# Kernel tuning notes

Measured on AMD Instinct MI355X. Metric: run time of the kernel, lower is better.

Reference implementation:

```python
import jax, jax.numpy as jnp
import numpy as np

B, S, H, NH = 4, 2048, 1024, 16
HD = H // NH
SCALE = 1.0 / np.sqrt(HD)
MASK_VAL = -1e9  # fp32 branch of the torch code


def setup_inputs() -> dict:
    key = jax.random.key(0)
    ks = jax.random.split(key, 6)
    s = 1.0 / np.sqrt(H)
    return {
        "x": jax.random.normal(ks[0], (B, S, H), dtype=jnp.float32),
        "attention_mask": jnp.ones((B, S), dtype=jnp.int32),
        "Wq": jax.random.normal(ks[1], (H, H), dtype=jnp.float32) * s,
        "Wk": jax.random.normal(ks[2], (H, H), dtype=jnp.float32) * s,
        "Wv": jax.random.normal(ks[3], (H, H), dtype=jnp.float32) * s,
        "Wo": jax.random.normal(ks[4], (H, H), dtype=jnp.float32) * s,
        "bo": jnp.zeros((H,), dtype=jnp.float32),
    }


def reference(x, attention_mask, Wq, Wk, Wv, Wo, bo):
    b, s, h = x.shape
    # projections; torch Linear computes x @ W.T
    q = (x @ Wq.T).reshape(b, s, NH, HD).transpose(0, 2, 1, 3)  # [b,nh,s,hd]
    k = (x @ Wk.T).reshape(b, s, NH, HD).transpose(0, 2, 1, 3)
    v = (x @ Wv.T).reshape(b, s, NH, HD).transpose(0, 2, 1, 3)

    scores = jnp.einsum("bhqd,bhkd->bhqk", q, k) * SCALE  # [b,nh,s,s]
    # padding mask: [b,1,1,s]
    pad = (attention_mask == 0)[:, None, None, :]
    scores = jnp.where(pad, MASK_VAL, scores)
    # causal mask
    causal = jnp.tril(jnp.ones((s, s), dtype=bool))[None, None]
    scores = jnp.where(causal, scores, MASK_VAL)

    attn = jax.nn.softmax(scores, axis=-1)  # dropout p=0 / eval -> identity
    out = jnp.einsum("bhqk,bhkd->bhqd", attn, v)
    out = out.transpose(0, 2, 1, 3).reshape(b, s, h)
    return out @ Wo.T + bo
```

## Files before the change

### kernel.cpp

```cpp
#include <hip/hip_runtime.h>

#define B_ 4
#define S_ 2048
#define H_ 1024
#define NH_ 16
#define HD_ 64
#define QSCALE_ 0.1803368801111204f

typedef __attribute__((ext_vector_type(8))) short bf16x8;
typedef __attribute__((ext_vector_type(4))) float f32x4;
typedef __attribute__((ext_vector_type(16))) float f32x16;

__device__ __forceinline__ unsigned short f2bf(float f) {
    unsigned u = __float_as_uint(f);
    unsigned r = (u + 0x7FFFu + ((u >> 16) & 1u)) >> 16;
    return (unsigned short)r;
}
__device__ __forceinline__ float exp2f_hw(float x) { return __builtin_amdgcn_exp2f(x); }

__global__ __launch_bounds__(256) void cast_f32_bf16(const float* __restrict__ in,
                                                     unsigned short* __restrict__ out, int n4) {
    int i = blockIdx.x * 256 + threadIdx.x;
    if (i < n4) {
        float4 v = reinterpret_cast<const float4*>(in)[i];
        ushort4 o;
        o.x = f2bf(v.x); o.y = f2bf(v.y); o.z = f2bf(v.z); o.w = f2bf(v.w);
        reinterpret_cast<ushort4*>(out)[i] = o;
    }
}

__device__ __forceinline__ void stage128_swz(const char* g, int gstride, char* lds, int tid) {
    int wave = tid >> 6, lane = tid & 63;
#pragma unroll
    for (int j = 0; j < 4; ++j) {
        int o = ((wave * 4 + j) * 64 + lane) * 16;
        int r = o >> 7;
        int slot = (o >> 4) & 7;
        const char* src = g + (size_t)r * gstride + ((slot ^ (r & 7)) << 4);
        __builtin_amdgcn_global_load_lds((const __attribute__((address_space(1))) void*)src,
                                         (__attribute__((address_space(3))) void*)(lds + (wave * 4 + j) * 1024),
                                         16, 0, 0);
    }
}
__device__ __forceinline__ void stage64_swz(const char* g, int gstride, char* lds, int tid) {
    int wave = tid >> 6, lane = tid & 63;
#pragma unroll
    for (int j = 0; j < 2; ++j) {
        int o = ((wave * 2 + j) * 64 + lane) * 16;
        int r = o >> 7;
        int slot = (o >> 4) & 7;
        const char* src = g + (size_t)r * gstride + ((slot ^ (r & 7)) << 4);
        __builtin_amdgcn_global_load_lds((const __attribute__((address_space(1))) void*)src,
                                         (__attribute__((address_space(3))) void*)(lds + (wave * 2 + j) * 1024),
                                         16, 0, 0);
    }
}

__device__ __forceinline__ bf16x8 frag_swz(const char* lds, int row, int slot) {
    return *reinterpret_cast<const bf16x8*>(lds + row * 128 + (((slot) ^ (row & 7)) << 4));
}

__global__ __launch_bounds__(256) void gemm_qkv(const unsigned short* __restrict__ xb,
                                                const unsigned short* __restrict__ Wq,
                                                const unsigned short* __restrict__ Wk,
                                                const unsigned short* __restrict__ Wv,
                                                unsigned short* __restrict__ Qo,
                                                unsigned short* __restrict__ Ko,
                                                unsigned short* __restrict__ Vo) {
    __shared__ __align__(16) char As[128 * 128];
    __shared__ __align__(16) char Bs[128 * 128];
    int tid = threadIdx.x, lane = tid & 63, wave = tid >> 6;
    int wr = wave >> 1, wc = wave & 1;
    int brow = blockIdx.x * 128;
    int mat = blockIdx.y >> 3;
    int bcol = (blockIdx.y & 7) * 128;
    const unsigned short* W = mat == 0 ? Wq : (mat == 1 ? Wk : Wv);
    unsigned short* O = mat == 0 ? Qo : (mat == 1 ? Ko : Vo);
    float oscale = (mat == 0) ? QSCALE_ : 1.0f;
    f32x4 acc[4][4] = {};
    const char* ga = (const char*)(xb + (size_t)brow * H_);
    const char* gb = (const char*)(W + (size_t)bcol * H_);
    int ro = lane & 15, kg = lane >> 4;
    for (int kt = 0; kt < H_ / 64; ++kt) {
        stage128_swz(ga + kt * 128, H_ * 2, As, tid);
        stage128_swz(gb + kt * 128, H_ * 2, Bs, tid);
        __syncthreads();
#pragma unroll
        for (int kk = 0; kk < 2; ++kk) {
            bf16x8 af[4], bfr[4];
#pragma unroll
            for (int m = 0; m < 4; ++m) af[m] = frag_swz(As, wr * 64 + m * 16 + ro, kk * 4 + kg);
#pragma unroll
            for (int n = 0; n < 4; ++n) bfr[n] = frag_swz(Bs, wc * 64 + n * 16 + ro, kk * 4 + kg);
#pragma unroll
            for (int m = 0; m < 4; ++m)
#pragma unroll
                for (int n = 0; n < 4; ++n)
                    acc[m][n] = __builtin_amdgcn_mfma_f32_16x16x32_bf16(af[m], bfr[n], acc[m][n], 0, 0, 0);
        }
        __syncthreads();
    }
#pragma unroll
    for (int m = 0; m < 4; ++m)
#pragma unroll
        for (int n = 0; n < 4; ++n)
#pragma unroll
            for (int i = 0; i < 4; ++i) {
                int row = brow + wr * 64 + m * 16 + kg * 4 + i;
                int col = bcol + wc * 64 + n * 16 + ro;
                O[(size_t)row * H_ + col] = f2bf(acc[m][n][i] * oscale);
            }
}

__global__ __launch_bounds__(256) void gemm_out(const unsigned short* __restrict__ Ab,
                                                const unsigned short* __restrict__ Wo,
                                                const float* __restrict__ bo,
                                                float* __restrict__ out) {
    __shared__ __align__(16) char As[128 * 128];
    __shared__ __align__(16) char Bs[128 * 128];
    int tid = threadIdx.x, lane = tid & 63, wave = tid >> 6;
    int wr = wave >> 1, wc = wave & 1;
    int brow = blockIdx.x * 128;
    int bcol = blockIdx.y * 128;
    f32x4 acc[4][4] = {};
    const char* ga = (const char*)(Ab + (size_t)brow * H_);
    const char* gb = (const char*)(Wo + (size_t)bcol * H_);
    int ro = lane & 15, kg = lane >> 4;
    for (int kt = 0; kt < H_ / 64; ++kt) {
        stage128_swz(ga + kt * 128, H_ * 2, As, tid);
        stage128_swz(gb + kt * 128, H_ * 2, Bs, tid);
        __syncthreads();
#pragma unroll
        for (int kk = 0; kk < 2; ++kk) {
            bf16x8 af[4], bfr[4];
#pragma unroll
            for (int m = 0; m < 4; ++m) af[m] = frag_swz(As, wr * 64 + m * 16 + ro, kk * 4 + kg);
#pragma unroll
            for (int n = 0; n < 4; ++n) bfr[n] = frag_swz(Bs, wc * 64 + n * 16 + ro, kk * 4 + kg);
#pragma unroll
            for (int m = 0; m < 4; ++m)
#pragma unroll
                for (int n = 0; n < 4; ++n)
                    acc[m][n] = __builtin_amdgcn_mfma_f32_16x16x32_bf16(af[m], bfr[n], acc[m][n], 0, 0, 0);
        }
        __syncthreads();
    }
#pragma unroll
    for (int n = 0; n < 4; ++n) {
        int col = bcol + wc * 64 + n * 16 + ro;
        float bn = bo[col];
#pragma unroll
        for (int m = 0; m < 4; ++m)
#pragma unroll
            for (int i = 0; i < 4; ++i) {
                int row = brow + wr * 64 + m * 16 + kg * 4 + i;
                out[(size_t)row * H_ + col] = acc[m][n][i] + bn;
            }
    }
}

__global__ __launch_bounds__(256) void attn(const unsigned short* __restrict__ Q,
                                            const unsigned short* __restrict__ K,
                                            const unsigned short* __restrict__ V,
                                            const int* __restrict__ amask,
                                            unsigned short* __restrict__ Ab) {
    __shared__ __align__(16) char Ksm[2 * 64 * 128];
    __shared__ __align__(16) unsigned short Vt[64 * 64];
    __shared__ unsigned char maskc[2048];
    __shared__ unsigned char anyz[32];

    int tid = threadIdx.x, lane = tid & 63, w = tid >> 6;
    int l31 = lane & 31, hi = lane >> 5, hi4 = hi * 4;
    int id = blockIdx.x;
    int qb = 15 - (id >> 6);
    int bh = id & 63, b = bh >> 4, h = bh & 15;
    int brow = qb * 128;
    int Qwg = brow + w * 32;

    unsigned cm = 0;
#pragma unroll
    for (int r = 0; r < 16; ++r)
        if (((r & 3) + 8 * (r >> 2) + hi4) > l31) cm |= (1u << r);

    {
        const int4* am4 = reinterpret_cast<const int4*>(amask + b * S_);
        for (int i = tid; i < S_ / 4; i += 256) {
            int4 v = am4[i];
            uchar4 o;
            o.x = (v.x == 0); o.y = (v.y == 0); o.z = (v.z == 0); o.w = (v.w == 0);
            reinterpret_cast<uchar4*>(maskc)[i] = o;
        }
    }
    __syncthreads();
    if (tid < 32) {
        const unsigned* mw = reinterpret_cast<const unsigned*>(maskc + tid * 64);
        unsigned o = 0;
#pragma unroll
        for (int i = 0; i < 16; ++i) o |= mw[i];
        anyz[tid] = o ? 1 : 0;
    }

    const unsigned short* Qg = Q + (size_t)(b * S_ + Qwg + l31) * H_ + h * HD_;
    const unsigned short* Kg = K + (size_t)b * S_ * H_ + h * HD_;
    const unsigned short* Vg = V + (size_t)b * S_ * H_ + h * HD_;

    bf16x8 qf[4];
#pragma unroll
    for (int kk = 0; kk < 4; ++kk)
        qf[kk] = *reinterpret_cast<const bf16x8*>(Qg + kk * 16 + hi * 8);

    stage64_swz((const char*)Kg, H_ * 2, Ksm, tid);
    bf16x8 vreg[2];
#pragma unroll
    for (int c = 0; c < 2; ++c) {
        int cid = c * 256 + tid;
        int r = cid & 63, d0 = (cid >> 6) * 8;
        vreg[c] = *reinterpret_cast<const bf16x8*>(Vg + (size_t)r * H_ + d0);
    }

    f32x16 oacc[2];
#pragma unroll
    for (int nd = 0; nd < 2; ++nd)
#pragma unroll
        for (int j = 0; j < 16; ++j) oacc[nd][j] = 0.f;
    float mrun = -__builtin_inff(), lrun = 0.f;

    int T = 2 * qb + 2;
    for (int t = 0; t < T; ++t) {
        int kv0 = t * 64;
        const char* Kc = Ksm + (t & 1) * 8192;

#pragma unroll
        for (int c = 0; c < 2; ++c) {
            int cid = c * 256 + tid;
            int r = cid & 63, d0 = (cid >> 6) * 8;
#pragma unroll
            for (int j = 0; j < 8; ++j) {
                int d = d0 + j;
                Vt[d * 64 + ((((r >> 3) ^ (d & 7)) << 3) | (r & 7))] = (unsigned short)vreg[c][j];
            }
        }
        __syncthreads();

        if (t + 1 < T)
            stage64_swz((const char*)(Kg + (size_t)(kv0 + 64) * H_), H_ * 2,
                        Ksm + ((t + 1) & 1) * 8192, tid);
        {
            int kvn = (t + 1 < T) ? kv0 + 64 : kv0;
#pragma unroll
            for (int c = 0; c < 2; ++c) {
                int cid = c * 256 + tid;
                int r = cid & 63, d0 = (cid >> 6) * 8;
                vreg[c] = *reinterpret_cast<const bf16x8*>(Vg + (size_t)(kvn + r) * H_ + d0);
            }
        }

        int c0 = kv0, c1 = kv0 + 32;
        if (c0 <= Qwg) {
            bool vis1 = (c1 <= Qwg);
            f32x16 sa[2];
#pragma unroll
            for (int n = 0; n < 2; ++n)
#pragma unroll
                for (int j = 0; j < 16; ++j) sa[n][j] = 0.f;

            __builtin_amdgcn_s_setprio(1);
#pragma unroll
            for (int kk = 0; kk < 4; ++kk) {
                bf16x8 kf0 = frag_swz(Kc, l31, 2 * kk + hi);
                sa[0] = __builtin_amdgcn_mfma_f32_32x32x16_bf16(kf0, qf[kk], sa[0], 0, 0, 0);
                if (vis1) {
                    bf16x8 kf1 = frag_swz(Kc, 32 + l31, 2 * kk + hi);
                    sa[1] = __builtin_amdgcn_mfma_f32_32x32x16_bf16(kf1, qf[kk], sa[1], 0, 0, 0);
                }
            }
            __builtin_amdgcn_s_setprio(0);

            if (c0 == Qwg) {
#pragma unroll
                for (int r = 0; r < 16; ++r)
                    sa[0][r] = (cm & (1u << r)) ? -1e9f : sa[0][r];
            }
            if (vis1 && c1 == Qwg) {
#pragma unroll
                for (int r = 0; r < 16; ++r)
                    sa[1][r] = (cm & (1u << r)) ? -1e9f : sa[1][r];
            }
            if (anyz[t]) {
#pragma unroll
                for (int n = 0; n < 2; ++n) {
                    if (n == 1 && !vis1) break;
#pragma unroll
                    for (int u = 0; u < 4; ++u) {
                        uchar4 mk = *reinterpret_cast<const uchar4*>(maskc + kv0 + 32 * n + 8 * u + hi4);
                        if (mk.x) sa[n][4 * u + 0] = -1e9f;
                        if (mk.y) sa[n][4 * u + 1] = -1e9f;
                        if (mk.z) sa[n][4 * u + 2] = -1e9f;
                        if (mk.w) sa[n][4 * u + 3] = -1e9f;
                    }
                }
            }

            float mx = -1e30f;
#pragma unroll
            for (int r = 0; r < 16; ++r) mx = fmaxf(mx, sa[0][r]);
            if (vis1) {
#pragma unroll
                for (int r = 0; r < 16; ++r) mx = fmaxf(mx, sa[1][r]);
            }
            mx = fmaxf(mx, __shfl_xor(mx, 32));

            bool grow = __any(mx > mrun);
            float mnew = fmaxf(mrun, mx);
            float fsc = 1.f;
            if (grow) {
                fsc = exp2f_hw(mrun - mnew);
                mrun = mnew;
#pragma unroll
                for (int nd = 0; nd < 2; ++nd)
#pragma unroll
                    for (int j = 0; j < 16; ++j) oacc[nd][j] *= fsc;
            }

            float rs = 0.f;
            __builtin_amdgcn_s_setprio(1);
#pragma unroll
            for (int n = 0; n < 2; ++n) {
                if (n == 1 && !vis1) break;
                unsigned int wrd[4][2];
#pragma unroll
                for (int u = 0; u < 4; ++u) {
                    float p0 = exp2f_hw(sa[n][4 * u + 0] - mnew);
                    float p1 = exp2f_hw(sa[n][4 * u + 1] - mnew);
                    float p2 = exp2f_hw(sa[n][4 * u + 2] - mnew);
                    float p3 = exp2f_hw(sa[n][4 * u + 3] - mnew);
                    rs += (p0 + p1) + (p2 + p3);
                    asm("v_cvt_pk_bf16_f32 %0, %1, %2" : "=v"(wrd[u][0]) : "v"(p0), "v"(p1));
                    asm("v_cvt_pk_bf16_f32 %0, %1, %2" : "=v"(wrd[u][1]) : "v"(p2), "v"(p3));
                }
#pragma unroll
                for (int half = 0; half < 2; ++half) {
                    int u0 = 2 * half;
                    unsigned int X0 = wrd[u0][0], Y0 = wrd[u0 + 1][0];
                    unsigned int X1 = wrd[u0][1], Y1 = wrd[u0 + 1][1];
                    asm("v_permlane32_swap_b32 %0, %1" : "+v"(X0), "+v"(Y0));
                    asm("v_permlane32_swap_b32 %0, %1" : "+v"(X1), "+v"(Y1));
                    union { unsigned int u[4]; bf16x8 v; } bu;
                    bu.u[0] = X0; bu.u[1] = X1; bu.u[2] = Y0; bu.u[3] = Y1;
                    int kc = 2 * n + half;
#pragma unroll
                    for (int nd = 0; nd < 2; ++nd) {
                        bf16x8 af = *reinterpret_cast<const bf16x8*>(
                            &Vt[(32 * nd + l31) * 64 + (((2 * kc + hi) ^ (l31 & 7)) << 3)]);
                        oacc[nd] = __builtin_amdgcn_mfma_f32_32x32x16_bf16(af, bu.v, oacc[nd], 0, 0, 0);
                    }
                }
            }
            __builtin_amdgcn_s_setprio(0);

            rs += __shfl_xor(rs, 32);
            lrun = lrun * fsc + rs;
        }
        __syncthreads();
    }

    float inv = 1.f / lrun;
    unsigned short* Osm = reinterpret_cast<unsigned short*>(Ksm);
#pragma unroll
    for (int nd = 0; nd < 2; ++nd)
#pragma unroll
        for (int r = 0; r < 16; ++r) {
            int d = 32 * nd + (r & 3) + 8 * (r >> 2) + hi4;
            Osm[w * 2048 + l31 * 64 + ((((d >> 3) ^ (l31 & 7)) << 3) | (d & 7))] =
                f2bf(oacc[nd][r] * inv);
        }
    __syncthreads();
#pragma unroll
    for (int wv = 0; wv < 4; ++wv) {
        int q = tid >> 3, j = tid & 7;
        bf16x8 vv = *reinterpret_cast<const bf16x8*>(Osm + wv * 2048 + q * 64 + ((j ^ (q & 7)) << 3));
        size_t row = (size_t)(b * S_ + brow + wv * 32 + q);
        *reinterpret_cast<bf16x8*>(Ab + row * H_ + h * HD_ + j * 8) = vv;
    }
}

extern "C" void kernel_launch(void* const* d_in, const int* in_sizes, int n_in,
                              void* d_out, int out_size, void* d_ws, size_t ws_size,
                              hipStream_t stream) {
    const float* x  = (const float*)d_in[0];
    const int* amask = (const int*)d_in[1];
    const float* Wq = (const float*)d_in[2];
    const float* Wk = (const float*)d_in[3];
    const float* Wv = (const float*)d_in[4];
    const float* Wo = (const float*)d_in[5];
    const float* bo = (const float*)d_in[6];
    float* out = (float*)d_out;

    const size_t XN = (size_t)B_ * S_ * H_;
    const size_t WN = (size_t)H_ * H_;

    char* ws = (char*)d_ws;
    unsigned short* xb  = (unsigned short*)ws;           ws += XN * 2;
    unsigned short* Wqb = (unsigned short*)ws;           ws += WN * 2;
    unsigned short* Wkb = (unsigned short*)ws;           ws += WN * 2;
    unsigned short* Wvb = (unsigned short*)ws;           ws += WN * 2;
    unsigned short* Wob = (unsigned short*)ws;           ws += WN * 2;
    unsigned short* Qb  = (unsigned short*)ws;           ws += XN * 2;
    unsigned short* Kb  = (unsigned short*)ws;           ws += XN * 2;
    unsigned short* Vb  = (unsigned short*)ws;           ws += XN * 2;
    unsigned short* Ab  = (unsigned short*)ws;           ws += XN * 2;

    cast_f32_bf16<<<(int)(XN / 4 / 256), 256, 0, stream>>>(x, xb, (int)(XN / 4));
    cast_f32_bf16<<<(int)(WN / 4 / 256), 256, 0, stream>>>(Wq, Wqb, (int)(WN / 4));
    cast_f32_bf16<<<(int)(WN / 4 / 256), 256, 0, stream>>>(Wk, Wkb, (int)(WN / 4));
    cast_f32_bf16<<<(int)(WN / 4 / 256), 256, 0, stream>>>(Wv, Wvb, (int)(WN / 4));
    cast_f32_bf16<<<(int)(WN / 4 / 256), 256, 0, stream>>>(Wo, Wob, (int)(WN / 4));

    gemm_qkv<<<dim3(64, 24), 256, 0, stream>>>(xb, Wqb, Wkb, Wvb, Qb, Kb, Vb);
    attn<<<1024, 256, 0, stream>>>(Qb, Kb, Vb, amask, Ab);
    gemm_out<<<dim3(64, 8), 256, 0, stream>>>(Ab, Wob, bo, out);
}
```

Baseline: 201.7 us.

## Fuse cast kernels, hoist attention loads, and use lazy softmax rescaling

Result: faster. 185.0 us (-8.3%).

```diff
diff --git a/kernel.cpp b/kernel.cpp
--- a/kernel.cpp
+++ b/kernel.cpp
@@ -18,15 +18,32 @@
 }
 __device__ __forceinline__ float exp2f_hw(float x) { return __builtin_amdgcn_exp2f(x); }
 
-__global__ __launch_bounds__(256) void cast_f32_bf16(const float* __restrict__ in,
-                                                     unsigned short* __restrict__ out, int n4) {
-    int i = blockIdx.x * 256 + threadIdx.x;
-    if (i < n4) {
-        float4 v = reinterpret_cast<const float4*>(in)[i];
-        ushort4 o;
-        o.x = f2bf(v.x); o.y = f2bf(v.y); o.z = f2bf(v.z); o.w = f2bf(v.w);
-        reinterpret_cast<ushort4*>(out)[i] = o;
-    }
+__global__ __launch_bounds__(256) void cast_all(const float* __restrict__ x,
+                                                const float* __restrict__ Wq,
+                                                const float* __restrict__ Wk,
+                                                const float* __restrict__ Wv,
+                                                const float* __restrict__ Wo,
+                                                unsigned short* __restrict__ xb,
+                                                unsigned short* __restrict__ Wqb,
+                                                unsigned short* __restrict__ Wkb,
+                                                unsigned short* __restrict__ Wvb,
+                                                unsigned short* __restrict__ Wob) {
+    int bid = blockIdx.x;
+    const float* src;
+    unsigned short* dst;
+    int i;
+    if (bid < 8192) {
+        src = x; dst = xb; i = bid * 256 + threadIdx.x;
+    } else {
+        int k = bid - 8192, wsel = k >> 10;
+        src = wsel == 0 ? Wq : wsel == 1 ? Wk : wsel == 2 ? Wv : Wo;
+        dst = wsel == 0 ? Wqb : wsel == 1 ? Wkb : wsel == 2 ? Wvb : Wob;
+        i = (k & 1023) * 256 + threadIdx.x;
+    }
+    float4 v = reinterpret_cast<const float4*>(src)[i];
+    ushort4 o;
+    o.x = f2bf(v.x); o.y = f2bf(v.y); o.z = f2bf(v.z); o.w = f2bf(v.w);
+    reinterpret_cast<ushort4*>(dst)[i] = o;
 }
 
 __device__ __forceinline__ void stage128_swz(const char* g, int gstride, char* lds, int tid) {
@@ -58,6 +75,15 @@
 
 __device__ __forceinline__ bf16x8 frag_swz(const char* lds, int row, int slot) {
     return *reinterpret_cast<const bf16x8*>(lds + row * 128 + (((slot) ^ (row & 7)) << 4));
+}
+
+__device__ __forceinline__ float vmax16(const f32x16& v) {
+    float a0 = fmaxf(v[0], v[1]), a1 = fmaxf(v[2], v[3]);
+    float a2 = fmaxf(v[4], v[5]), a3 = fmaxf(v[6], v[7]);
+    float a4 = fmaxf(v[8], v[9]), a5 = fmaxf(v[10], v[11]);
+    float a6 = fmaxf(v[12], v[13]), a7 = fmaxf(v[14], v[15]);
+    float b0 = fmaxf(a0, a1), b1 = fmaxf(a2, a3), b2 = fmaxf(a4, a5), b3 = fmaxf(a6, a7);
+    return fmaxf(fmaxf(b0, b1), fmaxf(b2, b3));
 }
 
 __global__ __launch_bounds__(256) void gemm_qkv(const unsigned short* __restrict__ xb,
@@ -182,6 +208,18 @@
     for (int r = 0; r < 16; ++r)
         if (((r & 3) + 8 * (r >> 2) + hi4) > l31) cm |= (1u << r);
 
+    const unsigned short* Qg = Q + (size_t)(b * S_ + Qwg + l31) * H_ + h * HD_;
+    const unsigned short* Kg = K + (size_t)b * S_ * H_ + h * HD_;
+    const unsigned short* Vg = V + (size_t)b * S_ * H_ + h * HD_;
+
+    stage64_swz((const char*)Kg, H_ * 2, Ksm, tid);
+    bf16x8 vreg[2];
+#pragma unroll
+    for (int c = 0; c < 2; ++c) {
+        int cid = c * 256 + tid;
+        int r = cid & 63, d0 = (cid >> 6) * 8;
+        vreg[c] = *reinterpret_cast<const bf16x8*>(Vg + (size_t)r * H_ + d0);
+    }
     {
         const int4* am4 = reinterpret_cast<const int4*>(amask + b * S_);
         for (int i = tid; i < S_ / 4; i += 256) {
@@ -191,6 +229,11 @@
             reinterpret_cast<uchar4*>(maskc)[i] = o;
         }
     }
+    bf16x8 qf[4];
+#pragma unroll
+    for (int kk = 0; kk < 4; ++kk)
+        qf[kk] = *reinterpret_cast<const bf16x8*>(Qg + kk * 16 + hi * 8);
+
     __syncthreads();
     if (tid < 32) {
         const unsigned* mw = reinterpret_cast<const unsigned*>(maskc + tid * 64);
@@ -200,29 +243,9 @@
         anyz[tid] = o ? 1 : 0;
     }
 
-    const unsigned short* Qg = Q + (size_t)(b * S_ + Qwg + l31) * H_ + h * HD_;
-    const unsigned short* Kg = K + (size_t)b * S_ * H_ + h * HD_;
-    const unsigned short* Vg = V + (size_t)b * S_ * H_ + h * HD_;
-
-    bf16x8 qf[4];
-#pragma unroll
-    for (int kk = 0; kk < 4; ++kk)
-        qf[kk] = *reinterpret_cast<const bf16x8*>(Qg + kk * 16 + hi * 8);
-
-    stage64_swz((const char*)Kg, H_ * 2, Ksm, tid);
-    bf16x8 vreg[2];
-#pragma unroll
-    for (int c = 0; c < 2; ++c) {
-        int cid = c * 256 + tid;
-        int r = cid & 63, d0 = (cid >> 6) * 8;
-        vreg[c] = *reinterpret_cast<const bf16x8*>(Vg + (size_t)r * H_ + d0);
-    }
-
-    f32x16 oacc[2];
-#pragma unroll
-    for (int nd = 0; nd < 2; ++nd)
-#pragma unroll
-        for (int j = 0; j < 16; ++j) oacc[nd][j] = 0.f;
+    f32x16 oacc0, oacc1;
+#pragma unroll
+    for (int j = 0; j < 16; ++j) { oacc0[j] = 0.f; oacc1[j] = 0.f; }
     float mrun = -__builtin_inff(), lrun = 0.f;
 
     int T = 2 * qb + 2;
@@ -234,11 +257,11 @@
         for (int c = 0; c < 2; ++c) {
             int cid = c * 256 + tid;
             int r = cid & 63, d0 = (cid >> 6) * 8;
-#pragma unroll
-            for (int j = 0; j < 8; ++j) {
-                int d = d0 + j;
-                Vt[d * 64 + ((((r >> 3) ^ (d & 7)) << 3) | (r & 7))] = (unsigned short)vreg[c][j];
-            }
+            unsigned short* vb = Vt + d0 * 64 + (r & 7);
+            int rs3 = (r >> 3) << 3;
+#pragma unroll
+            for (int j = 0; j < 8; ++j)
+                vb[j * 64 + (rs3 ^ (j << 3))] = (unsigned short)vreg[c][j];
         }
         __syncthreads();
 
@@ -258,68 +281,62 @@
         int c0 = kv0, c1 = kv0 + 32;
         if (c0 <= Qwg) {
             bool vis1 = (c1 <= Qwg);
-            f32x16 sa[2];
-#pragma unroll
-            for (int n = 0; n < 2; ++n)
-#pragma unroll
-                for (int j = 0; j < 16; ++j) sa[n][j] = 0.f;
+            f32x16 sa0, sa1;
+#pragma unroll
+            for (int j = 0; j < 16; ++j) { sa0[j] = 0.f; sa1[j] = 0.f; }
 
             __builtin_amdgcn_s_setprio(1);
 #pragma unroll
             for (int kk = 0; kk < 4; ++kk) {
                 bf16x8 kf0 = frag_swz(Kc, l31, 2 * kk + hi);
-                sa[0] = __builtin_amdgcn_mfma_f32_32x32x16_bf16(kf0, qf[kk], sa[0], 0, 0, 0);
+                sa0 = __builtin_amdgcn_mfma_f32_32x32x16_bf16(kf0, qf[kk], sa0, 0, 0, 0);
                 if (vis1) {
                     bf16x8 kf1 = frag_swz(Kc, 32 + l31, 2 * kk + hi);
-                    sa[1] = __builtin_amdgcn_mfma_f32_32x32x16_bf16(kf1, qf[kk], sa[1], 0, 0, 0);
+                    sa1 = __builtin_amdgcn_mfma_f32_32x32x16_bf16(kf1, qf[kk], sa1, 0, 0, 0);
                 }
             }
             __builtin_amdgcn_s_setprio(0);
 
             if (c0 == Qwg) {
 #pragma unroll
-                for (int r = 0; r < 16; ++r)
-                    sa[0][r] = (cm & (1u << r)) ? -1e9f : sa[0][r];
+                for (int r = 0; r < 16; ++r) sa0[r] = (cm & (1u << r)) ? -1e9f : sa0[r];
             }
             if (vis1 && c1 == Qwg) {
 #pragma unroll
-                for (int r = 0; r < 16; ++r)
-                    sa[1][r] = (cm & (1u << r)) ? -1e9f : sa[1][r];
+                for (int r = 0; r < 16; ++r) sa1[r] = (cm & (1u << r)) ? -1e9f : sa1[r];
             }
             if (anyz[t]) {
 #pragma unroll
-                for (int n = 0; n < 2; ++n) {
-                    if (n == 1 && !vis1) break;
+                for (int u = 0; u < 4; ++u) {
+                    uchar4 mk = *reinterpret_cast<const uchar4*>(maskc + kv0 + 8 * u + hi4);
+                    if (mk.x) sa0[4 * u + 0] = -1e9f;
+                    if (mk.y) sa0[4 * u + 1] = -1e9f;
+                    if (mk.z) sa0[4 * u + 2] = -1e9f;
+                    if (mk.w) sa0[4 * u + 3] = -1e9f;
+                }
+                if (vis1) {
 #pragma unroll
                     for (int u = 0; u < 4; ++u) {
-                        uchar4 mk = *reinterpret_cast<const uchar4*>(maskc + kv0 + 32 * n + 8 * u + hi4);
-                        if (mk.x) sa[n][4 * u + 0] = -1e9f;
-                        if (mk.y) sa[n][4 * u + 1] = -1e9f;
-                        if (mk.z) sa[n][4 * u + 2] = -1e9f;
-                        if (mk.w) sa[n][4 * u + 3] = -1e9f;
+                        uchar4 mk = *reinterpret_cast<const uchar4*>(maskc + kv0 + 32 + 8 * u + hi4);
+                        if (mk.x) sa1[4 * u + 0] = -1e9f;
+                        if (mk.y) sa1[4 * u + 1] = -1e9f;
+                        if (mk.z) sa1[4 * u + 2] = -1e9f;
+                        if (mk.w) sa1[4 * u + 3] = -1e9f;
                     }
                 }
             }
 
-            float mx = -1e30f;
-#pragma unroll
-            for (int r = 0; r < 16; ++r) mx = fmaxf(mx, sa[0][r]);
-            if (vis1) {
-#pragma unroll
-                for (int r = 0; r < 16; ++r) mx = fmaxf(mx, sa[1][r]);
-            }
+            float mx = vmax16(sa0);
+            if (vis1) mx = fmaxf(mx, vmax16(sa1));
             mx = fmaxf(mx, __shfl_xor(mx, 32));
 
-            bool grow = __any(mx > mrun);
-            float mnew = fmaxf(mrun, mx);
-            float fsc = 1.f;
-            if (grow) {
-                fsc = exp2f_hw(mrun - mnew);
+            if (__any(mx > mrun + 10.f)) {
+                float mnew = fmaxf(mrun, mx);
+                float fsc = exp2f_hw(mrun - mnew);
                 mrun = mnew;
-#pragma unroll
-                for (int nd = 0; nd < 2; ++nd)
-#pragma unroll
-                    for (int j = 0; j < 16; ++j) oacc[nd][j] *= fsc;
+                lrun *= fsc;
+#pragma unroll
+                for (int j = 0; j < 16; ++j) { oacc0[j] *= fsc; oacc1[j] *= fsc; }
             }
 
             float rs = 0.f;
@@ -327,13 +344,14 @@
 #pragma unroll
             for (int n = 0; n < 2; ++n) {
                 if (n == 1 && !vis1) break;
+                const f32x16& sa = (n == 0) ? sa0 : sa1;
                 unsigned int wrd[4][2];
 #pragma unroll
                 for (int u = 0; u < 4; ++u) {
-                    float p0 = exp2f_hw(sa[n][4 * u + 0] - mnew);
-                    float p1 = exp2f_hw(sa[n][4 * u + 1] - mnew);
-                    float p2 = exp2f_hw(sa[n][4 * u + 2] - mnew);
-                    float p3 = exp2f_hw(sa[n][4 * u + 3] - mnew);
+                    float p0 = exp2f_hw(sa[4 * u + 0] - mrun);
+                    float p1 = exp2f_hw(sa[4 * u + 1] - mrun);
+                    float p2 = exp2f_hw(sa[4 * u + 2] - mrun);
+                    float p3 = exp2f_hw(sa[4 * u + 3] - mrun);
                     rs += (p0 + p1) + (p2 + p3);
                     asm("v_cvt_pk_bf16_f32 %0, %1, %2" : "=v"(wrd[u][0]) : "v"(p0), "v"(p1));
                     asm("v_cvt_pk_bf16_f32 %0, %1, %2" : "=v"(wrd[u][1]) : "v"(p2), "v"(p3));
@@ -348,18 +366,18 @@
                     union { unsigned int u[4]; bf16x8 v; } bu;
                     bu.u[0] = X0; bu.u[1] = X1; bu.u[2] = Y0; bu.u[3] = Y1;
                     int kc = 2 * n + half;
-#pragma unroll
-                    for (int nd = 0; nd < 2; ++nd) {
-                        bf16x8 af = *reinterpret_cast<const bf16x8*>(
-                            &Vt[(32 * nd + l31) * 64 + (((2 * kc + hi) ^ (l31 & 7)) << 3)]);
-                        oacc[nd] = __builtin_amdgcn_mfma_f32_32x32x16_bf16(af, bu.v, oacc[nd], 0, 0, 0);
-                    }
+                    bf16x8 af0 = *reinterpret_cast<const bf16x8*>(
+                        &Vt[(l31) * 64 + (((2 * kc + hi) ^ (l31 & 7)) << 3)]);
+                    oacc0 = __builtin_amdgcn_mfma_f32_32x32x16_bf16(af0, bu.v, oacc0, 0, 0, 0);
+                    bf16x8 af1 = *reinterpret_cast<const bf16x8*>(
+                        &Vt[(32 + l31) * 64 + (((2 * kc + hi) ^ (l31 & 7)) << 3)]);
+                    oacc1 = __builtin_amdgcn_mfma_f32_32x32x16_bf16(af1, bu.v, oacc1, 0, 0, 0);
                 }
             }
             __builtin_amdgcn_s_setprio(0);
 
             rs += __shfl_xor(rs, 32);
-            lrun = lrun * fsc + rs;
+            lrun += rs;
         }
         __syncthreads();
     }
@@ -367,13 +385,12 @@
     float inv = 1.f / lrun;
     unsigned short* Osm = reinterpret_cast<unsigned short*>(Ksm);
 #pragma unroll
-    for (int nd = 0; nd < 2; ++nd)
-#pragma unroll
-        for (int r = 0; r < 16; ++r) {
-            int d = 32 * nd + (r & 3) + 8 * (r >> 2) + hi4;
-            Osm[w * 2048 + l31 * 64 + ((((d >> 3) ^ (l31 & 7)) << 3) | (d & 7))] =
-                f2bf(oacc[nd][r] * inv);
-        }
+    for (int r = 0; r < 16; ++r) {
+        int d = (r & 3) + 8 * (r >> 2) + hi4;
+        Osm[w * 2048 + l31 * 64 + ((((d >> 3) ^ (l31 & 7)) << 3) | (d & 7))] = f2bf(oacc0[r] * inv);
+        int d1 = d + 32;
+        Osm[w * 2048 + l31 * 64 + ((((d1 >> 3) ^ (l31 & 7)) << 3) | (d1 & 7))] = f2bf(oacc1[r] * inv);
+    }
     __syncthreads();
 #pragma unroll
     for (int wv = 0; wv < 4; ++wv) {
@@ -410,12 +427,7 @@
     unsigned short* Vb  = (unsigned short*)ws;           ws += XN * 2;
     unsigned short* Ab  = (unsigned short*)ws;           ws += XN * 2;
 
-    cast_f32_bf16<<<(int)(XN / 4 / 256), 256, 0, stream>>>(x, xb, (int)(XN / 4));
-    cast_f32_bf16<<<(int)(WN / 4 / 256), 256, 0, stream>>>(Wq, Wqb, (int)(WN / 4));
-    cast_f32_bf16<<<(int)(WN / 4 / 256), 256, 0, stream>>>(Wk, Wkb, (int)(WN / 4));
-    cast_f32_bf16<<<(int)(WN / 4 / 256), 256, 0, stream>>>(Wv, Wvb, (int)(WN / 4));
-    cast_f32_bf16<<<(int)(WN / 4 / 256), 256, 0, stream>>>(Wo, Wob, (int)(WN / 4));
-
+    cast_all<<<12288, 256, 0, stream>>>(x, Wq, Wk, Wv, Wo, xb, Wqb, Wkb, Wvb, Wob);
     gemm_qkv<<<dim3(64, 24), 256, 0, stream>>>(xb, Wqb, Wkb, Wvb, Qb, Kb, Vb);
     attn<<<1024, 256, 0, stream>>>(Qb, Kb, Vb, amask, Ab);
     gemm_out<<<dim3(64, 8), 256, 0, stream>>>(Ab, Wob, bo, out);
```
